# Kernel optimization log

Measured on AMD Instinct MI355X. Metric: run time of the kernel, lower is better.

The kernel has to match this reference:

```python
import jax, jax.numpy as jnp
import numpy as np

IN_FEATURES = 4096
OUT_FEATURES = 11008
BATCH = 2048


def setup_inputs() -> dict:
    key = jax.random.key(0)
    k1, k2, k3, k4 = jax.random.split(key, 4)
    # int8-range activations, stored as int32 for exact integer accumulation
    input = jax.random.randint(k1, (BATCH, IN_FEATURES), -127, 128, dtype=jnp.int32)
    # ternary weights in {-1, 0, 1}
    ternary_weight = jax.random.randint(k2, (OUT_FEATURES, IN_FEATURES), -1, 2, dtype=jnp.int32)
    weight_scale = jax.random.uniform(k3, (OUT_FEATURES, 1), dtype=jnp.float32, minval=0.01, maxval=0.1)
    bias = jax.random.normal(k4, (OUT_FEATURES,), dtype=jnp.float32) * 0.01
    return {"input": input, "ternary_weight": ternary_weight,
            "weight_scale": weight_scale, "bias": bias}


def reference(input, ternary_weight, weight_scale, bias):
    # Equivalent to the per-column add/sub loop: int32 accumulate of
    # input @ ternary_weight.T, since w in {-1,0,1}.
    acc = jnp.einsum('bi,oi->bo', input, ternary_weight)  # int32 [B, O]
    out = acc.astype(jnp.float32) * weight_scale.reshape(1, -1)
    out = out + bias
    return out
```

## Files before the change

### kernel.cpp

```cpp
#include <hip/hip_runtime.h>
#include <stdint.h>

#define BATCH   2048
#define KDIM    4096
#define NDIM    11008

#define BM 128
#define BN 256
#define BK 64
#define NT (KDIM / BK)
#define ABYTES (BM * BK)
#define BBYTES (BN * BK)
#define BUF_BYTES (ABYTES + BBYTES)
#define A_OFF 0
#define B_OFF ABYTES

typedef __attribute__((ext_vector_type(4))) int i32x4;

typedef const __attribute__((address_space(1))) char glob_char;
typedef __attribute__((address_space(3))) char lds_char;

__device__ __forceinline__ unsigned pack4(i32x4 v) {
  return  ((unsigned)v.x & 0xFFu)
        | (((unsigned)v.y & 0xFFu) << 8)
        | (((unsigned)v.z & 0xFFu) << 16)
        | (((unsigned)v.w)         << 24);
}

__global__ __launch_bounds__(256) void convert_i32_i8(const int* __restrict__ src,
                                                      unsigned* __restrict__ dst,
                                                      int n4) {
  int idx = blockIdx.x * 256 + threadIdx.x;
  if (idx >= n4) return;
  i32x4 v = ((const i32x4*)src)[idx];
  dst[idx] = pack4(v);
}

__global__ __launch_bounds__(256, 2) void ternary_gemm(const char* __restrict__ A8,
                                                       const char* __restrict__ B8,
                                                       const float* __restrict__ scale,
                                                       const float* __restrict__ bias,
                                                       float* __restrict__ out) {
  __shared__ char lds[3 * BUF_BYTES];

  const int tid  = threadIdx.x;
  const int wid  = tid >> 6;
  const int lane = tid & 63;

  const int wg  = (blockIdx.x & 7) * 86 + (blockIdx.x >> 3);
  const int mtq = wg / 172;
  const int r   = wg - mtq * 172;
  const int nt  = r >> 2;
  const int mt  = mtq * 4 + (r & 3);
  const int arow0 = mt * BM;
  const int brow0 = nt * BN;

  const int wr = wid >> 1;
  const int wc = wid & 1;
  const int rsub = lane & 15;
  const int sgrp = lane >> 4;

  const int srow  = tid >> 2;
  const int sslot = (tid & 3) ^ ((srow >> 1) & 3);
  const char* gA0 = A8 + (size_t)(arow0       + srow) * KDIM + sslot * 16;
  const char* gA1 = A8 + (size_t)(arow0 +  64 + srow) * KDIM + sslot * 16;
  const char* gB0 = B8 + (size_t)(brow0       + srow) * KDIM + sslot * 16;
  const char* gB1 = B8 + (size_t)(brow0 +  64 + srow) * KDIM + sslot * 16;
  const char* gB2 = B8 + (size_t)(brow0 + 128 + srow) * KDIM + sslot * 16;
  const char* gB3 = B8 + (size_t)(brow0 + 192 + srow) * KDIM + sslot * 16;

  auto stage = [&](const char* g, int bufo, int kt, int dsto) {
    __builtin_amdgcn_global_load_lds((glob_char*)(g + kt * BK),
        (lds_char*)(lds + bufo + dsto + wid * 1024), 16, 0, 0);
  };
  auto stage_tile = [&](int bufo, int kt) {
    stage(gA0, bufo, kt, A_OFF);
    stage(gA1, bufo, kt, A_OFF + 4096);
    stage(gB0, bufo, kt, B_OFF);
    stage(gB1, bufo, kt, B_OFF + 4096);
    stage(gB2, bufo, kt, B_OFF + 8192);
    stage(gB3, bufo, kt, B_OFF + 12288);
  };

  int offA[4], offB[8];
#pragma unroll
  for (int m = 0; m < 4; ++m) {
    const int row = wr * 64 + m * 16 + rsub;
    const int p   = sgrp ^ ((row >> 1) & 3);
    offA[m] = A_OFF + row * 64 + p * 16;
  }
#pragma unroll
  for (int n = 0; n < 8; ++n) {
    const int row = wc * 128 + n * 16 + rsub;
    const int p   = sgrp ^ ((row >> 1) & 3);
    offB[n] = B_OFF + row * 64 + p * 16;
  }

  i32x4 acc[4][8];
#pragma unroll
  for (int m = 0; m < 4; ++m)
#pragma unroll
    for (int n = 0; n < 8; ++n)
      acc[m][n] = (i32x4){0, 0, 0, 0};

  int cur = 0, nxt = BUF_BYTES, pf = 2 * BUF_BYTES;

  stage_tile(cur, 0);
  stage_tile(nxt, 1);
  asm volatile("s_waitcnt vmcnt(6)" ::: "memory");
  __builtin_amdgcn_s_barrier();

  for (int t = 0; t < NT; ++t) {
    const int kt2 = (t + 2 < NT) ? t + 2 : NT - 1;

    stage_tile(pf, kt2);

    i32x4 a0 = *(const i32x4*)(lds + cur + offA[0]);
    i32x4 a1 = *(const i32x4*)(lds + cur + offA[1]);
    i32x4 a2 = *(const i32x4*)(lds + cur + offA[2]);
    i32x4 a3 = *(const i32x4*)(lds + cur + offA[3]);
    i32x4 b0 = *(const i32x4*)(lds + cur + offB[0]);
    i32x4 b1 = *(const i32x4*)(lds + cur + offB[1]);
    i32x4 b2 = *(const i32x4*)(lds + cur + offB[2]);
    i32x4 b3 = *(const i32x4*)(lds + cur + offB[3]);
    i32x4 b4 = *(const i32x4*)(lds + cur + offB[4]);
    i32x4 b5 = *(const i32x4*)(lds + cur + offB[5]);
    i32x4 b6 = *(const i32x4*)(lds + cur + offB[6]);
    i32x4 b7 = *(const i32x4*)(lds + cur + offB[7]);

    __builtin_amdgcn_s_setprio(1);
    acc[0][0] = __builtin_amdgcn_mfma_i32_16x16x64_i8(a0, b0, acc[0][0], 0, 0, 0);
    acc[1][0] = __builtin_amdgcn_mfma_i32_16x16x64_i8(a1, b0, acc[1][0], 0, 0, 0);
    acc[2][0] = __builtin_amdgcn_mfma_i32_16x16x64_i8(a2, b0, acc[2][0], 0, 0, 0);
    acc[3][0] = __builtin_amdgcn_mfma_i32_16x16x64_i8(a3, b0, acc[3][0], 0, 0, 0);
    acc[0][1] = __builtin_amdgcn_mfma_i32_16x16x64_i8(a0, b1, acc[0][1], 0, 0, 0);
    acc[1][1] = __builtin_amdgcn_mfma_i32_16x16x64_i8(a1, b1, acc[1][1], 0, 0, 0);
    acc[2][1] = __builtin_amdgcn_mfma_i32_16x16x64_i8(a2, b1, acc[2][1], 0, 0, 0);
    acc[3][1] = __builtin_amdgcn_mfma_i32_16x16x64_i8(a3, b1, acc[3][1], 0, 0, 0);
    acc[0][2] = __builtin_amdgcn_mfma_i32_16x16x64_i8(a0, b2, acc[0][2], 0, 0, 0);
    acc[1][2] = __builtin_amdgcn_mfma_i32_16x16x64_i8(a1, b2, acc[1][2], 0, 0, 0);
    acc[2][2] = __builtin_amdgcn_mfma_i32_16x16x64_i8(a2, b2, acc[2][2], 0, 0, 0);
    acc[3][2] = __builtin_amdgcn_mfma_i32_16x16x64_i8(a3, b2, acc[3][2], 0, 0, 0);
    acc[0][3] = __builtin_amdgcn_mfma_i32_16x16x64_i8(a0, b3, acc[0][3], 0, 0, 0);
    acc[1][3] = __builtin_amdgcn_mfma_i32_16x16x64_i8(a1, b3, acc[1][3], 0, 0, 0);
    acc[2][3] = __builtin_amdgcn_mfma_i32_16x16x64_i8(a2, b3, acc[2][3], 0, 0, 0);
    acc[3][3] = __builtin_amdgcn_mfma_i32_16x16x64_i8(a3, b3, acc[3][3], 0, 0, 0);
    acc[0][4] = __builtin_amdgcn_mfma_i32_16x16x64_i8(a0, b4, acc[0][4], 0, 0, 0);
    acc[1][4] = __builtin_amdgcn_mfma_i32_16x16x64_i8(a1, b4, acc[1][4], 0, 0, 0);
    acc[2][4] = __builtin_amdgcn_mfma_i32_16x16x64_i8(a2, b4, acc[2][4], 0, 0, 0);
    acc[3][4] = __builtin_amdgcn_mfma_i32_16x16x64_i8(a3, b4, acc[3][4], 0, 0, 0);
    acc[0][5] = __builtin_amdgcn_mfma_i32_16x16x64_i8(a0, b5, acc[0][5], 0, 0, 0);
    acc[1][5] = __builtin_amdgcn_mfma_i32_16x16x64_i8(a1, b5, acc[1][5], 0, 0, 0);
    acc[2][5] = __builtin_amdgcn_mfma_i32_16x16x64_i8(a2, b5, acc[2][5], 0, 0, 0);
    acc[3][5] = __builtin_amdgcn_mfma_i32_16x16x64_i8(a3, b5, acc[3][5], 0, 0, 0);
    acc[0][6] = __builtin_amdgcn_mfma_i32_16x16x64_i8(a0, b6, acc[0][6], 0, 0, 0);
    acc[1][6] = __builtin_amdgcn_mfma_i32_16x16x64_i8(a1, b6, acc[1][6], 0, 0, 0);
    acc[2][6] = __builtin_amdgcn_mfma_i32_16x16x64_i8(a2, b6, acc[2][6], 0, 0, 0);
    acc[3][6] = __builtin_amdgcn_mfma_i32_16x16x64_i8(a3, b6, acc[3][6], 0, 0, 0);
    acc[0][7] = __builtin_amdgcn_mfma_i32_16x16x64_i8(a0, b7, acc[0][7], 0, 0, 0);
    acc[1][7] = __builtin_amdgcn_mfma_i32_16x16x64_i8(a1, b7, acc[1][7], 0, 0, 0);
    acc[2][7] = __builtin_amdgcn_mfma_i32_16x16x64_i8(a2, b7, acc[2][7], 0, 0, 0);
    acc[3][7] = __builtin_amdgcn_mfma_i32_16x16x64_i8(a3, b7, acc[3][7], 0, 0, 0);
    __builtin_amdgcn_s_setprio(0);

    asm volatile("s_waitcnt vmcnt(6)" ::: "memory");
    __builtin_amdgcn_s_barrier();

    const int tb = cur; cur = nxt; nxt = pf; pf = tb;
  }

  const int crow = sgrp * 4;
#pragma unroll
  for (int n = 0; n < 8; ++n) {
    const int col = brow0 + wc * 128 + n * 16 + rsub;
    const float sc = scale[col];
    const float bs = bias[col];
#pragma unroll
    for (int m = 0; m < 4; ++m) {
      const int r0 = arow0 + wr * 64 + m * 16 + crow;
#pragma unroll
      for (int j = 0; j < 4; ++j) {
        out[(size_t)(r0 + j) * NDIM + col] = (float)acc[m][n][j] * sc + bs;
      }
    }
  }
}

extern "C" void kernel_launch(void* const* d_in, const int* in_sizes, int n_in,
                              void* d_out, int out_size, void* d_ws, size_t ws_size,
                              hipStream_t stream) {
  const int*   input  = (const int*)d_in[0];
  const int*   weight = (const int*)d_in[1];
  const float* scale  = (const float*)d_in[2];
  const float* bias   = (const float*)d_in[3];
  float*       out    = (float*)d_out;

  const size_t needA = (size_t)BATCH * KDIM;
  const size_t needB = (size_t)NDIM * KDIM;

  char* A8 = (char*)d_ws;
  char* B8 = A8 + needA;
  const int nA4 = (int)(needA / 4);
  const int nB4 = (int)(needB / 4);
  convert_i32_i8<<<(nA4 + 255) / 256, 256, 0, stream>>>(input, (unsigned*)A8, nA4);
  convert_i32_i8<<<(nB4 + 255) / 256, 256, 0, stream>>>(weight, (unsigned*)B8, nB4);

  const dim3 grid((BATCH / BM) * (NDIM / BN));
  const dim3 block(256);
  ternary_gemm<<<grid, block, 0, stream>>>(A8, B8, scale, bias, out);
  (void)ws_size; (void)n_in; (void)in_sizes; (void)out_size;
}
```

Before: 155.7 us.

## Enlarge GEMM tile to 256x256 with 512-thread blocks and simpler block mapping

Doubles the M tile to 256 rows and the workgroup to 8 waves in a 2x4 arrangement, so each wave computes 128x64 instead of 64x128. Staging and LDS offsets are adjusted so each thread issues 4 global-to-LDS loads per K step, and the wait counts change to match. The grouped/swizzled block-to-tile mapping is replaced by a plain mt = blockIdx&7 mapping. The intent is more operand reuse per byte loaded and less global traffic, at the cost of a larger LDS footprint (3 buffers of 32KB), fewer blocks (344), and possibly worse L2 locality and occupancy.

```diff
diff --git a/kernel.cpp b/kernel.cpp
--- a/kernel.cpp
+++ b/kernel.cpp
@@ -5,7 +5,7 @@
 #define KDIM    4096
 #define NDIM    11008
 
-#define BM 128
+#define BM 256
 #define BN 256
 #define BK 64
 #define NT (KDIM / BK)
@@ -36,7 +36,7 @@
   dst[idx] = pack4(v);
 }
 
-__global__ __launch_bounds__(256, 2) void ternary_gemm(const char* __restrict__ A8,
+__global__ __launch_bounds__(512, 2) void ternary_gemm(const char* __restrict__ A8,
                                                        const char* __restrict__ B8,
                                                        const float* __restrict__ scale,
                                                        const float* __restrict__ bias,
@@ -47,27 +47,22 @@
   const int wid  = tid >> 6;
   const int lane = tid & 63;
 
-  const int wg  = (blockIdx.x & 7) * 86 + (blockIdx.x >> 3);
-  const int mtq = wg / 172;
-  const int r   = wg - mtq * 172;
-  const int nt  = r >> 2;
-  const int mt  = mtq * 4 + (r & 3);
+  const int mt = blockIdx.x & 7;
+  const int nt = blockIdx.x >> 3;
   const int arow0 = mt * BM;
   const int brow0 = nt * BN;
 
-  const int wr = wid >> 1;
-  const int wc = wid & 1;
+  const int wr = wid >> 2;
+  const int wc = wid & 3;
   const int rsub = lane & 15;
   const int sgrp = lane >> 4;
 
   const int srow  = tid >> 2;
   const int sslot = (tid & 3) ^ ((srow >> 1) & 3);
   const char* gA0 = A8 + (size_t)(arow0       + srow) * KDIM + sslot * 16;
-  const char* gA1 = A8 + (size_t)(arow0 +  64 + srow) * KDIM + sslot * 16;
+  const char* gA1 = A8 + (size_t)(arow0 + 128 + srow) * KDIM + sslot * 16;
   const char* gB0 = B8 + (size_t)(brow0       + srow) * KDIM + sslot * 16;
-  const char* gB1 = B8 + (size_t)(brow0 +  64 + srow) * KDIM + sslot * 16;
-  const char* gB2 = B8 + (size_t)(brow0 + 128 + srow) * KDIM + sslot * 16;
-  const char* gB3 = B8 + (size_t)(brow0 + 192 + srow) * KDIM + sslot * 16;
+  const char* gB1 = B8 + (size_t)(brow0 + 128 + srow) * KDIM + sslot * 16;
 
   auto stage = [&](const char* g, int bufo, int kt, int dsto) {
     __builtin_amdgcn_global_load_lds((glob_char*)(g + kt * BK),
@@ -75,39 +70,37 @@
   };
   auto stage_tile = [&](int bufo, int kt) {
     stage(gA0, bufo, kt, A_OFF);
-    stage(gA1, bufo, kt, A_OFF + 4096);
+    stage(gA1, bufo, kt, A_OFF + 8192);
     stage(gB0, bufo, kt, B_OFF);
-    stage(gB1, bufo, kt, B_OFF + 4096);
-    stage(gB2, bufo, kt, B_OFF + 8192);
-    stage(gB3, bufo, kt, B_OFF + 12288);
+    stage(gB1, bufo, kt, B_OFF + 8192);
   };
 
-  int offA[4], offB[8];
-#pragma unroll
-  for (int m = 0; m < 4; ++m) {
-    const int row = wr * 64 + m * 16 + rsub;
+  int offA[8], offB[4];
+#pragma unroll
+  for (int m = 0; m < 8; ++m) {
+    const int row = wr * 128 + m * 16 + rsub;
     const int p   = sgrp ^ ((row >> 1) & 3);
     offA[m] = A_OFF + row * 64 + p * 16;
   }
 #pragma unroll
-  for (int n = 0; n < 8; ++n) {
-    const int row = wc * 128 + n * 16 + rsub;
+  for (int n = 0; n < 4; ++n) {
+    const int row = wc * 64 + n * 16 + rsub;
     const int p   = sgrp ^ ((row >> 1) & 3);
     offB[n] = B_OFF + row * 64 + p * 16;
   }
 
-  i32x4 acc[4][8];
-#pragma unroll
-  for (int m = 0; m < 4; ++m)
-#pragma unroll
-    for (int n = 0; n < 8; ++n)
+  i32x4 acc[8][4];
+#pragma unroll
+  for (int m = 0; m < 8; ++m)
+#pragma unroll
+    for (int n = 0; n < 4; ++n)
       acc[m][n] = (i32x4){0, 0, 0, 0};
 
   int cur = 0, nxt = BUF_BYTES, pf = 2 * BUF_BYTES;
 
   stage_tile(cur, 0);
   stage_tile(nxt, 1);
-  asm volatile("s_waitcnt vmcnt(6)" ::: "memory");
+  asm volatile("s_waitcnt vmcnt(4)" ::: "memory");
   __builtin_amdgcn_s_barrier();
 
   for (int t = 0; t < NT; ++t) {
@@ -119,51 +112,51 @@
     i32x4 a1 = *(const i32x4*)(lds + cur + offA[1]);
     i32x4 a2 = *(const i32x4*)(lds + cur + offA[2]);
     i32x4 a3 = *(const i32x4*)(lds + cur + offA[3]);
+    i32x4 a4 = *(const i32x4*)(lds + cur + offA[4]);
+    i32x4 a5 = *(const i32x4*)(lds + cur + offA[5]);
+    i32x4 a6 = *(const i32x4*)(lds + cur + offA[6]);
+    i32x4 a7 = *(const i32x4*)(lds + cur + offA[7]);
     i32x4 b0 = *(const i32x4*)(lds + cur + offB[0]);
     i32x4 b1 = *(const i32x4*)(lds + cur + offB[1]);
     i32x4 b2 = *(const i32x4*)(lds + cur + offB[2]);
     i32x4 b3 = *(const i32x4*)(lds + cur + offB[3]);
-    i32x4 b4 = *(const i32x4*)(lds + cur + offB[4]);
-    i32x4 b5 = *(const i32x4*)(lds + cur + offB[5]);
-    i32x4 b6 = *(const i32x4*)(lds + cur + offB[6]);
-    i32x4 b7 = *(const i32x4*)(lds + cur + offB[7]);
 
     __builtin_amdgcn_s_setprio(1);
     acc[0][0] = __builtin_amdgcn_mfma_i32_16x16x64_i8(a0, b0, acc[0][0], 0, 0, 0);
     acc[1][0] = __builtin_amdgcn_mfma_i32_16x16x64_i8(a1, b0, acc[1][0], 0, 0, 0);
     acc[2][0] = __builtin_amdgcn_mfma_i32_16x16x64_i8(a2, b0, acc[2][0], 0, 0, 0);
     acc[3][0] = __builtin_amdgcn_mfma_i32_16x16x64_i8(a3, b0, acc[3][0], 0, 0, 0);
+    acc[4][0] = __builtin_amdgcn_mfma_i32_16x16x64_i8(a4, b0, acc[4][0], 0, 0, 0);
+    acc[5][0] = __builtin_amdgcn_mfma_i32_16x16x64_i8(a5, b0, acc[5][0], 0, 0, 0);
+    acc[6][0] = __builtin_amdgcn_mfma_i32_16x16x64_i8(a6, b0, acc[6][0], 0, 0, 0);
+    acc[7][0] = __builtin_amdgcn_mfma_i32_16x16x64_i8(a7, b0, acc[7][0], 0, 0, 0);
     acc[0][1] = __builtin_amdgcn_mfma_i32_16x16x64_i8(a0, b1, acc[0][1], 0, 0, 0);
     acc[1][1] = __builtin_amdgcn_mfma_i32_16x16x64_i8(a1, b1, acc[1][1], 0, 0, 0);
     acc[2][1] = __builtin_amdgcn_mfma_i32_16x16x64_i8(a2, b1, acc[2][1], 0, 0, 0);
     acc[3][1] = __builtin_amdgcn_mfma_i32_16x16x64_i8(a3, b1, acc[3][1], 0, 0, 0);
+    acc[4][1] = __builtin_amdgcn_mfma_i32_16x16x64_i8(a4, b1, acc[4][1], 0, 0, 0);
+    acc[5][1] = __builtin_amdgcn_mfma_i32_16x16x64_i8(a5, b1, acc[5][1], 0, 0, 0);
+    acc[6][1] = __builtin_amdgcn_mfma_i32_16x16x64_i8(a6, b1, acc[6][1], 0, 0, 0);
+    acc[7][1] = __builtin_amdgcn_mfma_i32_16x16x64_i8(a7, b1, acc[7][1], 0, 0, 0);
     acc[0][2] = __builtin_amdgcn_mfma_i32_16x16x64_i8(a0, b2, acc[0][2], 0, 0, 0);
     acc[1][2] = __builtin_amdgcn_mfma_i32_16x16x64_i8(a1, b2, acc[1][2], 0, 0, 0);
     acc[2][2] = __builtin_amdgcn_mfma_i32_16x16x64_i8(a2, b2, acc[2][2], 0, 0, 0);
     acc[3][2] = __builtin_amdgcn_mfma_i32_16x16x64_i8(a3, b2, acc[3][2], 0, 0, 0);
+    acc[4][2] = __builtin_amdgcn_mfma_i32_16x16x64_i8(a4, b2, acc[4][2], 0, 0, 0);
+    acc[5][2] = __builtin_amdgcn_mfma_i32_16x16x64_i8(a5, b2, acc[5][2], 0, 0, 0);
+    acc[6][2] = __builtin_amdgcn_mfma_i32_16x16x64_i8(a6, b2, acc[6][2], 0, 0, 0);
+    acc[7][2] = __builtin_amdgcn_mfma_i32_16x16x64_i8(a7, b2, acc[7][2], 0, 0, 0);
     acc[0][3] = __builtin_amdgcn_mfma_i32_16x16x64_i8(a0, b3, acc[0][3], 0, 0, 0);
     acc[1][3] = __builtin_amdgcn_mfma_i32_16x16x64_i8(a1, b3, acc[1][3], 0, 0, 0);
     acc[2][3] = __builtin_amdgcn_mfma_i32_16x16x64_i8(a2, b3, acc[2][3], 0, 0, 0);
     acc[3][3] = __builtin_amdgcn_mfma_i32_16x16x64_i8(a3, b3, acc[3][3], 0, 0, 0);
-    acc[0][4] = __builtin_amdgcn_mfma_i32_16x16x64_i8(a0, b4, acc[0][4], 0, 0, 0);
-    acc[1][4] = __builtin_amdgcn_mfma_i32_16x16x64_i8(a1, b4, acc[1][4], 0, 0, 0);
-    acc[2][4] = __builtin_amdgcn_mfma_i32_16x16x64_i8(a2, b4, acc[2][4], 0, 0, 0);
-    acc[3][4] = __builtin_amdgcn_mfma_i32_16x16x64_i8(a3, b4, acc[3][4], 0, 0, 0);
-    acc[0][5] = __builtin_amdgcn_mfma_i32_16x16x64_i8(a0, b5, acc[0][5], 0, 0, 0);
-    acc[1][5] = __builtin_amdgcn_mfma_i32_16x16x64_i8(a1, b5, acc[1][5], 0, 0, 0);
-    acc[2][5] = __builtin_amdgcn_mfma_i32_16x16x64_i8(a2, b5, acc[2][5], 0, 0, 0);
-    acc[3][5] = __builtin_amdgcn_mfma_i32_16x16x64_i8(a3, b5, acc[3][5], 0, 0, 0);
-    acc[0][6] = __builtin_amdgcn_mfma_i32_16x16x64_i8(a0, b6, acc[0][6], 0, 0, 0);
-    acc[1][6] = __builtin_amdgcn_mfma_i32_16x16x64_i8(a1, b6, acc[1][6], 0, 0, 0);
-    acc[2][6] = __builtin_amdgcn_mfma_i32_16x16x64_i8(a2, b6, acc[2][6], 0, 0, 0);
-    acc[3][6] = __builtin_amdgcn_mfma_i32_16x16x64_i8(a3, b6, acc[3][6], 0, 0, 0);
-    acc[0][7] = __builtin_amdgcn_mfma_i32_16x16x64_i8(a0, b7, acc[0][7], 0, 0, 0);
-    acc[1][7] = __builtin_amdgcn_mfma_i32_16x16x64_i8(a1, b7, acc[1][7], 0, 0, 0);
-    acc[2][7] = __builtin_amdgcn_mfma_i32_16x16x64_i8(a2, b7, acc[2][7], 0, 0, 0);
-    acc[3][7] = __builtin_amdgcn_mfma_i32_16x16x64_i8(a3, b7, acc[3][7], 0, 0, 0);
+    acc[4][3] = __builtin_amdgcn_mfma_i32_16x16x64_i8(a4, b3, acc[4][3], 0, 0, 0);
+    acc[5][3] = __builtin_amdgcn_mfma_i32_16x16x64_i8(a5, b3, acc[5][3], 0, 0, 0);
+    acc[6][3] = __builtin_amdgcn_mfma_i32_16x16x64_i8(a6, b3, acc[6][3], 0, 0, 0);
+    acc[7][3] = __builtin_amdgcn_mfma_i32_16x16x64_i8(a7, b3, acc[7][3], 0, 0, 0);
     __builtin_amdgcn_s_setprio(0);
 
-    asm volatile("s_waitcnt vmcnt(6)" ::: "memory");
+    asm volatile("s_waitcnt vmcnt(4)" ::: "memory");
     __builtin_amdgcn_s_barrier();
 
     const int tb = cur; cur = nxt; nxt = pf; pf = tb;
@@ -171,13 +164,13 @@
 
   const int crow = sgrp * 4;
 #pragma unroll
-  for (int n = 0; n < 8; ++n) {
-    const int col = brow0 + wc * 128 + n * 16 + rsub;
+  for (int n = 0; n < 4; ++n) {
+    const int col = brow0 + wc * 64 + n * 16 + rsub;
     const float sc = scale[col];
     const float bs = bias[col];
 #pragma unroll
-    for (int m = 0; m < 4; ++m) {
-      const int r0 = arow0 + wr * 64 + m * 16 + crow;
+    for (int m = 0; m < 8; ++m) {
+      const int r0 = arow0 + wr * 128 + m * 16 + crow;
 #pragma unroll
       for (int j = 0; j < 4; ++j) {
         out[(size_t)(r0 + j) * NDIM + col] = (float)acc[m][n][j] * sc + bs;
@@ -206,7 +199,7 @@
   convert_i32_i8<<<(nB4 + 255) / 256, 256, 0, stream>>>(weight, (unsigned*)B8, nB4);
 
   const dim3 grid((BATCH / BM) * (NDIM / BN));
-  const dim3 block(256);
+  const dim3 block(512);
   ternary_gemm<<<grid, block, 0, stream>>>(A8, B8, scale, bias, out);
   (void)ws_size; (void)n_in; (void)in_sizes; (void)out_size;
 }
```

Result: slower. 167.8 us (+7.8%).
